# Kernel tuning notes

Measured on AMD Instinct MI355X. Metric: run time of the kernel, lower is better.

The kernel has to match this reference:

```python
import jax, jax.numpy as jnp
import numpy as np

S, E, H, V = 2048, 1024, 1024, 32000


def setup_inputs() -> dict:
    key = jax.random.key(0)
    ks = jax.random.split(key, 12)
    def n(k, shape, s=0.02):
        return jax.random.normal(k, shape, dtype=jnp.float32) * s
    return {
        "encoder_out": n(ks[0], (S, E), 1.0),
        "word_input": jax.random.randint(ks[1], (1,), 0, V),
        "last_context": n(ks[2], (1, H), 1.0),
        "h0": jnp.zeros((1, 1, H), jnp.float32),
        "c0": jnp.zeros((1, 1, H), jnp.float32),
        "emb": n(ks[3], (V, E)),
        "W_ih": n(ks[4], (4 * H, E + H)),
        "b_ih": jnp.zeros((4 * H,), jnp.float32),
        "W_hh": n(ks[5], (4 * H, H)),
        "b_hh": jnp.zeros((4 * H,), jnp.float32),
        "W_att": n(ks[6], (H, E + H)),
        "b_att": jnp.zeros((H,), jnp.float32),
        "v": jax.random.uniform(ks[7], (H,), dtype=jnp.float32) * 0.1,
        "W_ah": n(ks[8], (H, E + H)),
        "b_ah": jnp.zeros((H,), jnp.float32),
        "W_out": n(ks[9], (V, H)),
        "b_out": jnp.zeros((V,), jnp.float32),
    }


def reference(encoder_out, word_input, last_context, h0, c0, emb,
              W_ih, b_ih, W_hh, b_hh, W_att, b_att, v, W_ah, b_ah,
              W_out, b_out):
    # --- single LSTM step (torch gate order: i, f, g, o) ---
    x_emb = emb[word_input[0]]                         # [E]
    lstm_in = jnp.concatenate([last_context[0], x_emb])  # [E+H]
    gates = W_ih @ lstm_in + b_ih + W_hh @ h0[0, 0] + b_hh  # [4H]
    i, f, g, o = jnp.split(gates, 4)
    i = jax.nn.sigmoid(i); f = jax.nn.sigmoid(f)
    g = jnp.tanh(g);       o = jax.nn.sigmoid(o)
    c = f * c0[0, 0] + i * g                           # [H]
    h = o * jnp.tanh(c)                                # [H] (dropout: eval = identity)

    # --- batched additive (Bahdanau-style) attention over all S steps ---
    cat = jnp.concatenate([jnp.broadcast_to(h[None, :], (S, H)), encoder_out], axis=1)  # [S, H+E]
    scores = jnp.tanh(cat @ W_att.T + b_att) @ v       # [S]
    w = jax.nn.softmax(scores)                         # [S]
    context = w @ encoder_out                          # [E]

    # --- output projection ---
    x_t = jnp.tanh(W_ah @ jnp.concatenate([context, h]) + b_ah)  # [H]
    output = jax.nn.log_softmax(W_out @ x_t + b_out)[None, :]    # [1, V]
    return (output, (h[None, None, :], c[None, None, :]), x_t[None, :], w[None, :])
```

## Files before the change

kernel.cpp:

```cpp
#include <hip/hip_runtime.h>
#include <math.h>

typedef unsigned short u16;
typedef unsigned int u32;

typedef float  floatx4 __attribute__((ext_vector_type(4)));
typedef short  shortx8 __attribute__((ext_vector_type(8)));

#define S_LEN 2048
#define E_DIM 1024
#define H_DIM 1024
#define V_DIM 32000

#define OUT_LOG 0
#define OUT_H   32000
#define OUT_C   33024
#define OUT_XT  34048
#define OUT_W   35072

#define WS_UB     0
#define WS_SCORES 1024
#define WS_CTX    3072
#define WS_EXPSUM 4097
#define WS_ENC16  4608
#define WS_W16    (4608 + 1048576)

__device__ __forceinline__ u16 f2bf_fast(float f) {
    union { float f; u32 i; } v; v.f = f;
    return (u16)((v.i + 0x8000u) >> 16);
}
__device__ __forceinline__ float red16_sum(float x) {
    #pragma unroll
    for (int m = 1; m <= 8; m <<= 1) x += __shfl_xor(x, m, 64);
    return x;
}
__device__ __forceinline__ float wave_sum(float x) {
    #pragma unroll
    for (int m = 32; m >= 1; m >>= 1) x += __shfl_xor(x, m, 64);
    return x;
}
__device__ __forceinline__ float wave_max(float x) {
    #pragma unroll
    for (int m = 32; m >= 1; m >>= 1) x = fmaxf(x, __shfl_xor(x, m, 64));
    return x;
}
__device__ __forceinline__ float dot4(float4 a, float4 b) {
    return a.x * b.x + a.y * b.y + a.z * b.z + a.w * b.w;
}
__device__ __forceinline__ void cvt8(u16* t, float4 a, float4 b) {
    t[0] = f2bf_fast(a.x); t[1] = f2bf_fast(a.y);
    t[2] = f2bf_fast(a.z); t[3] = f2bf_fast(a.w);
    t[4] = f2bf_fast(b.x); t[5] = f2bf_fast(b.y);
    t[6] = f2bf_fast(b.z); t[7] = f2bf_fast(b.w);
}

__global__ __launch_bounds__(256) void k_lstm(
    const float* __restrict__ last_ctx, const int* __restrict__ word,
    const float* __restrict__ emb, const float* __restrict__ h0,
    const float* __restrict__ c0,
    const float* __restrict__ W_ih, const float* __restrict__ b_ih,
    const float* __restrict__ W_hh, const float* __restrict__ b_hh,
    float* __restrict__ out_h, float* __restrict__ out_c)
{
    __shared__ float gsh[4];
    int tid = threadIdx.x;
    int g = tid >> 6, l = tid & 63;
    int j = blockIdx.x;
    int row = g * H_DIM + j;
    const float* embrow = emb + (size_t)word[0] * E_DIM;
    const float* wrow = W_ih + (size_t)row * (E_DIM + H_DIM);
    const float* hrow = W_hh + (size_t)row * H_DIM;
    int c4 = l * 4;

    float s = 0.f;
    #pragma unroll
    for (int it = 0; it < 4; ++it) {
        int col = it * 256 + c4;
        s += dot4(*(const float4*)(wrow + col), *(const float4*)(last_ctx + col));
    }
    #pragma unroll
    for (int it = 0; it < 4; ++it) {
        int col = it * 256 + c4;
        s += dot4(*(const float4*)(wrow + 1024 + col), *(const float4*)(embrow + col));
    }
    #pragma unroll
    for (int it = 0; it < 4; ++it) {
        int col = it * 256 + c4;
        s += dot4(*(const float4*)(hrow + col), *(const float4*)(h0 + col));
    }
    s = wave_sum(s);
    if (l == 0) gsh[g] = s + b_ih[row] + b_hh[row];
    __syncthreads();
    if (tid == 0) {
        float gi = 1.f / (1.f + expf(-gsh[0]));
        float gf = 1.f / (1.f + expf(-gsh[1]));
        float gg = tanhf(gsh[2]);
        float go = 1.f / (1.f + expf(-gsh[3]));
        float c = gf * c0[j] + gi * gg;
        float h = go * tanhf(c);
        out_h[j] = h;
        out_c[j] = c;
    }
}

__global__ __launch_bounds__(256) void k_uproj(
    const float* __restrict__ W_att, const float* __restrict__ b_att,
    const float* __restrict__ out_h, const float* __restrict__ enc,
    float* __restrict__ wsf)
{
    int tid = threadIdx.x;
    int b = blockIdx.x;
    int gid = b * 256 + tid;
    if (gid < S_LEN) wsf[WS_SCORES + gid] = 0.f;
    else if (gid < S_LEN + E_DIM) wsf[WS_CTX + gid - S_LEN] = 0.f;
    else if (gid == S_LEN + E_DIM) wsf[WS_EXPSUM] = 0.f;

    int w = tid >> 6, l = tid & 63;
    int r = b * 4 + w;
    const float* wrow = W_att + (size_t)r * (E_DIM + H_DIM);
    int c4 = l * 4;
    float s = 0.f;
    #pragma unroll
    for (int it = 0; it < 4; ++it) {
        int col = it * 256 + c4;
        s += dot4(*(const float4*)(wrow + col), *(const float4*)(out_h + col));
    }
    s = wave_sum(s);
    if (l == 0) wsf[WS_UB + r] = s + b_att[r];

    u16* enc16 = (u16*)(wsf + WS_ENC16);
    u16* w16   = (u16*)(wsf + WS_W16);
    {
        int row = b * 8 + (tid >> 5);
        int col = (tid & 31) * 32;
        const float* src = enc + (size_t)row * E_DIM + col;
        u16 t[32];
        #pragma unroll
        for (int m = 0; m < 32; m += 8) {
            float4 x = *(const float4*)(src + m);
            float4 y = *(const float4*)(src + m + 4);
            cvt8(t + m, x, y);
        }
        uint4* dst = (uint4*)(enc16 + (size_t)row * E_DIM + col);
        #pragma unroll
        for (int m = 0; m < 4; ++m) dst[m] = *(uint4*)(t + m * 8);
    }
    {
        int row = b * 4 + (tid >> 6);
        int col = (tid & 63) * 16;
        const float* src = W_att + (size_t)row * (E_DIM + H_DIM) + H_DIM + col;
        u16 t[16];
        float4 x0 = *(const float4*)(src);
        float4 x1 = *(const float4*)(src + 4);
        float4 x2 = *(const float4*)(src + 8);
        float4 x3 = *(const float4*)(src + 12);
        cvt8(t, x0, x1); cvt8(t + 8, x2, x3);
        uint4* dst = (uint4*)(w16 + (size_t)row * E_DIM + col);
        dst[0] = *(uint4*)(t);
        dst[1] = *(uint4*)(t + 8);
    }
}

#define LDS_P 40
__global__ __launch_bounds__(256) void k_att_scores(
    const u16* __restrict__ enc16, const u16* __restrict__ w16,
    const float* __restrict__ vvec, const float* __restrict__ ws_ub,
    float* __restrict__ ws_scores)
{
    __shared__ u16 lds_a[2][64 * LDS_P];
    __shared__ u16 lds_b[2][64 * LDS_P];

    int tid = threadIdx.x;
    int w = tid >> 6, l = tid & 63;
    int b = blockIdx.x;
    int s0 = (b & 31) * 64;
    int r0 = (b >> 5) * 64;
    int lrow = l & 15, lq = l >> 4;

    int half = tid >> 7;
    int t128 = tid & 127;
    int srow = t128 >> 1;
    int scol = (t128 & 1) * 16;
    const u16* pbase = half == 0
        ? enc16 + (size_t)(s0 + srow) * E_DIM + scol
        : w16   + (size_t)(r0 + srow) * E_DIM + scol;
    u16* dst[2];
    dst[0] = half == 0 ? &lds_a[0][srow * LDS_P + scol] : &lds_b[0][srow * LDS_P + scol];
    dst[1] = half == 0 ? &lds_a[1][srow * LDS_P + scol] : &lds_b[1][srow * LDS_P + scol];

    floatx4 acc[4];
    #pragma unroll
    for (int i = 0; i < 4; ++i) acc[i] = (floatx4)0.f;

    {
        uint4 v0 = *(const uint4*)(pbase);
        uint4 v1 = *(const uint4*)(pbase + 8);
        *(uint4*)(dst[0])     = v0;
        *(uint4*)(dst[0] + 8) = v1;
    }
    __syncthreads();

    int cur = 0;
    for (int kc = 0; kc < 32; ++kc) {
        uint4 n0, n1;
        if (kc < 31) {
            const u16* p = pbase + (kc + 1) * 32;
            n0 = *(const uint4*)(p);
            n1 = *(const uint4*)(p + 8);
        }

        shortx8 afrag = *(const shortx8*)&lds_a[cur][(w * 16 + lrow) * LDS_P + lq * 8];
        #pragma unroll
        for (int rc = 0; rc < 4; ++rc) {
            shortx8 bfrag = *(const shortx8*)&lds_b[cur][(rc * 16 + lrow) * LDS_P + lq * 8];
            acc[rc] = __builtin_amdgcn_mfma_f32_16x16x32_bf16(afrag, bfrag, acc[rc], 0, 0, 0);
        }

        if (kc < 31) {
            int nb = cur ^ 1;
            *(uint4*)(dst[nb])     = n0;
            *(uint4*)(dst[nb] + 8) = n1;
        }
        __syncthreads();
        cur ^= 1;
    }

    float part[4] = {0.f, 0.f, 0.f, 0.f};
    #pragma unroll
    for (int rc = 0; rc < 4; ++rc) {
        int r = r0 + rc * 16 + lrow;
        float ubr = ws_ub[r];
        float vr  = vvec[r];
        #pragma unroll
        for (int reg = 0; reg < 4; ++reg)
            part[reg] += tanhf(acc[rc][reg] + ubr) * vr;
    }
    #pragma unroll
    for (int m = 1; m <= 8; m <<= 1)
        #pragma unroll
        for (int reg = 0; reg < 4; ++reg)
            part[reg] += __shfl_xor(part[reg], m, 64);
    if (lrow == 0) {
        int sbase = s0 + w * 16 + lq * 4;
        #pragma unroll
        for (int reg = 0; reg < 4; ++reg)
            atomicAdd(&ws_scores[sbase + reg], part[reg]);
    }
}

__global__ __launch_bounds__(256) void k_ctx(
    const float* __restrict__ enc, const float* __restrict__ ws_scores,
    float* __restrict__ out_w, float* __restrict__ ws_ctx)
{
    __shared__ float red[4];
    __shared__ float w_lds[16];
    __shared__ float bM, bS;
    int tid = threadIdx.x, b = blockIdx.x;

    float4 sa = *(const float4*)(ws_scores + tid * 8);
    float4 sb = *(const float4*)(ws_scores + tid * 8 + 4);
    float m = fmaxf(fmaxf(fmaxf(sa.x, sa.y), fmaxf(sa.z, sa.w)),
                    fmaxf(fmaxf(sb.x, sb.y), fmaxf(sb.z, sb.w)));
    m = wave_max(m);
    if ((tid & 63) == 0) red[tid >> 6] = m;
    __syncthreads();
    if (tid == 0) bM = fmaxf(fmaxf(red[0], red[1]), fmaxf(red[2], red[3]));
    __syncthreads();
    float M = bM;
    float e = expf(sa.x - M) + expf(sa.y - M) + expf(sa.z - M) + expf(sa.w - M)
            + expf(sb.x - M) + expf(sb.y - M) + expf(sb.z - M) + expf(sb.w - M);
    e = wave_sum(e);
    if ((tid & 63) == 0) red[tid >> 6] = e;
    __syncthreads();
    if (tid == 0) bS = red[0] + red[1] + red[2] + red[3];
    __syncthreads();
    float inv = 1.f / bS;

    int sbase = b * 16;
    if (tid < 16) {
        float wt = expf(ws_scores[sbase + tid] - M) * inv;
        w_lds[tid] = wt;
        out_w[sbase + tid] = wt;
    }
    __syncthreads();

    int e4 = tid * 4;
    float a0 = 0.f, a1 = 0.f, a2 = 0.f, a3 = 0.f;
    #pragma unroll 4
    for (int i = 0; i < 16; ++i) {
        float wt = w_lds[i];
        float4 ev = *(const float4*)(enc + (size_t)(sbase + i) * E_DIM + e4);
        a0 += wt * ev.x; a1 += wt * ev.y; a2 += wt * ev.z; a3 += wt * ev.w;
    }
    atomicAdd(&ws_ctx[e4 + 0], a0);
    atomicAdd(&ws_ctx[e4 + 1], a1);
    atomicAdd(&ws_ctx[e4 + 2], a2);
    atomicAdd(&ws_ctx[e4 + 3], a3);
}

__global__ __launch_bounds__(256) void k_xt(
    const float* __restrict__ W_ah, const float* __restrict__ b_ah,
    const float* __restrict__ ws_ctx, const float* __restrict__ out_h,
    float* __restrict__ out_xt)
{
    int tid = threadIdx.x;
    int w = tid >> 6, l = tid & 63;
    int r = blockIdx.x * 4 + w;
    const float* wrow = W_ah + (size_t)r * (E_DIM + H_DIM);
    int c4 = l * 4;
    float s = 0.f;
    #pragma unroll
    for (int it = 0; it < 4; ++it) {
        int col = it * 256 + c4;
        s += dot4(*(const float4*)(wrow + col), *(const float4*)(ws_ctx + col));
        s += dot4(*(const float4*)(wrow + 1024 + col), *(const float4*)(out_h + col));
    }
    s = wave_sum(s);
    if (l == 0) out_xt[r] = tanhf(s + b_ah[r]);
}

__global__ __launch_bounds__(256) void k_logits(
    const float* __restrict__ W_out, const float* __restrict__ b_out,
    const float* __restrict__ out_xt,
    float* __restrict__ out_log, float* __restrict__ ws_expsum)
{
    __shared__ float red[4];
    int tid = threadIdx.x;
    int w = tid >> 6, l = tid & 63;
    int sub = l >> 4, l16 = l & 15;
    int row = blockIdx.x * 16 + w * 4 + sub;
    const float* wrow = W_out + (size_t)row * H_DIM;
    int c4 = l16 * 4;
    float s = 0.f;
    #pragma unroll 4
    for (int it = 0; it < 16; ++it) {
        int col = it * 64 + c4;
        s += dot4(*(const float4*)(wrow + col), *(const float4*)(out_xt + col));
    }
    s = red16_sum(s);
    float lg = s + b_out[row];
    float e = 0.f;
    if (l16 == 0) { out_log[row] = lg; e = expf(lg); }
    e = wave_sum(e);
    if (l == 0) red[w] = e;
    __syncthreads();
    if (tid == 0)
        atomicAdd(ws_expsum, red[0] + red[1] + red[2] + red[3]);
}

__global__ __launch_bounds__(256) void k_writeout(
    const float* __restrict__ ws_expsum, float* __restrict__ out_log)
{
    int i = blockIdx.x * 256 + threadIdx.x;
    float lz = logf(ws_expsum[0]);
    out_log[i] = out_log[i] - lz;
}

extern "C" void kernel_launch(void* const* d_in, const int* in_sizes, int n_in,
                              void* d_out, int out_size, void* d_ws, size_t ws_size,
                              hipStream_t stream) {
    const float* enc      = (const float*)d_in[0];
    const int*   word     = (const int*)d_in[1];
    const float* last_ctx = (const float*)d_in[2];
    const float* h0       = (const float*)d_in[3];
    const float* c0       = (const float*)d_in[4];
    const float* emb      = (const float*)d_in[5];
    const float* W_ih     = (const float*)d_in[6];
    const float* b_ih     = (const float*)d_in[7];
    const float* W_hh     = (const float*)d_in[8];
    const float* b_hh     = (const float*)d_in[9];
    const float* W_att    = (const float*)d_in[10];
    const float* b_att    = (const float*)d_in[11];
    const float* vvec     = (const float*)d_in[12];
    const float* W_ah     = (const float*)d_in[13];
    const float* b_ah     = (const float*)d_in[14];
    const float* W_out    = (const float*)d_in[15];
    const float* b_out    = (const float*)d_in[16];

    float* wsf = (float*)d_ws;

    float* out     = (float*)d_out;
    float* out_log = out + OUT_LOG;
    float* out_h   = out + OUT_H;
    float* out_c   = out + OUT_C;
    float* out_xt  = out + OUT_XT;
    float* out_w   = out + OUT_W;

    k_lstm<<<1024, 256, 0, stream>>>(last_ctx, word, emb, h0, c0,
                                     W_ih, b_ih, W_hh, b_hh, out_h, out_c);
    k_uproj<<<256, 256, 0, stream>>>(W_att, b_att, out_h, enc, wsf);
    k_att_scores<<<512, 256, 0, stream>>>((const u16*)(wsf + WS_ENC16),
                                          (const u16*)(wsf + WS_W16),
                                          vvec, wsf + WS_UB, wsf + WS_SCORES);
    k_ctx<<<128, 256, 0, stream>>>(enc, wsf + WS_SCORES, out_w, wsf + WS_CTX);
    k_xt<<<256, 256, 0, stream>>>(W_ah, b_ah, wsf + WS_CTX, out_h, out_xt);
    k_logits<<<2000, 256, 0, stream>>>(W_out, b_out, out_xt,
                                       out_log, wsf + WS_EXPSUM);
    k_writeout<<<125, 256, 0, stream>>>(wsf + WS_EXPSUM, out_log);
}
```

Measured before the change: 360.0 us.

## Move bf16 conversion into LSTM kernel and replace score atomics with partial buffers

The fp32-to-bf16 conversion of encoder_out and the W_att encoder slice moves from k_uproj into k_lstm, spreading it across 1024 blocks that are already reading weights. In k_att_scores, the per-row-block score partials are written to a [16, S] buffer instead of being accumulated with atomicAdd. k_ctx then sums the 16 partials itself, which also removes the need to zero the scores buffer. This trades atomic contention for extra partial-buffer reads in every k_ctx block.

```diff
diff --git a/kernel.cpp b/kernel.cpp
--- a/kernel.cpp
+++ b/kernel.cpp
@@ -19,11 +19,11 @@
 #define OUT_W   35072
 
 #define WS_UB     0
-#define WS_SCORES 1024
-#define WS_CTX    3072
-#define WS_EXPSUM 4097
-#define WS_ENC16  4608
-#define WS_W16    (4608 + 1048576)
+#define WS_CTX    1024
+#define WS_EXPSUM 2048
+#define WS_PART   2560
+#define WS_ENC16  35840
+#define WS_W16    (35840 + 1048576)
 
 __device__ __forceinline__ u16 f2bf_fast(float f) {
     union { float f; u32 i; } v; v.f = f;
@@ -60,7 +60,9 @@
     const float* __restrict__ c0,
     const float* __restrict__ W_ih, const float* __restrict__ b_ih,
     const float* __restrict__ W_hh, const float* __restrict__ b_hh,
-    float* __restrict__ out_h, float* __restrict__ out_c)
+    const float* __restrict__ W_att, const float* __restrict__ enc,
+    float* __restrict__ out_h, float* __restrict__ out_c,
+    float* __restrict__ wsf)
 {
     __shared__ float gsh[4];
     int tid = threadIdx.x;
@@ -90,6 +92,29 @@
     }
     s = wave_sum(s);
     if (l == 0) gsh[g] = s + b_ih[row] + b_hh[row];
+
+    u16* enc16 = (u16*)(wsf + WS_ENC16);
+    u16* w16   = (u16*)(wsf + WS_W16);
+    {
+        int prow = 2 * j + (tid >> 7);
+        int pcol = (tid & 127) * 8;
+        const float* src = enc + (size_t)prow * E_DIM + pcol;
+        float4 x = *(const float4*)(src);
+        float4 y = *(const float4*)(src + 4);
+        u16 t[8];
+        cvt8(t, x, y);
+        *(uint4*)(enc16 + (size_t)prow * E_DIM + pcol) = *(uint4*)t;
+    }
+    {
+        int pcol = tid * 4;
+        const float* src = W_att + (size_t)j * (E_DIM + H_DIM) + H_DIM + pcol;
+        float4 x = *(const float4*)(src);
+        u16 t[4];
+        t[0] = f2bf_fast(x.x); t[1] = f2bf_fast(x.y);
+        t[2] = f2bf_fast(x.z); t[3] = f2bf_fast(x.w);
+        *(uint2*)(w16 + (size_t)j * E_DIM + pcol) = *(uint2*)t;
+    }
+
     __syncthreads();
     if (tid == 0) {
         float gi = 1.f / (1.f + expf(-gsh[0]));
@@ -105,15 +130,13 @@
 
 __global__ __launch_bounds__(256) void k_uproj(
     const float* __restrict__ W_att, const float* __restrict__ b_att,
-    const float* __restrict__ out_h, const float* __restrict__ enc,
-    float* __restrict__ wsf)
+    const float* __restrict__ out_h, float* __restrict__ wsf)
 {
     int tid = threadIdx.x;
     int b = blockIdx.x;
     int gid = b * 256 + tid;
-    if (gid < S_LEN) wsf[WS_SCORES + gid] = 0.f;
-    else if (gid < S_LEN + E_DIM) wsf[WS_CTX + gid - S_LEN] = 0.f;
-    else if (gid == S_LEN + E_DIM) wsf[WS_EXPSUM] = 0.f;
+    if (gid < E_DIM) wsf[WS_CTX + gid] = 0.f;
+    else if (gid == E_DIM) wsf[WS_EXPSUM] = 0.f;
 
     int w = tid >> 6, l = tid & 63;
     int r = b * 4 + w;
@@ -127,45 +150,13 @@
     }
     s = wave_sum(s);
     if (l == 0) wsf[WS_UB + r] = s + b_att[r];
-
-    u16* enc16 = (u16*)(wsf + WS_ENC16);
-    u16* w16   = (u16*)(wsf + WS_W16);
-    {
-        int row = b * 8 + (tid >> 5);
-        int col = (tid & 31) * 32;
-        const float* src = enc + (size_t)row * E_DIM + col;
-        u16 t[32];
-        #pragma unroll
-        for (int m = 0; m < 32; m += 8) {
-            float4 x = *(const float4*)(src + m);
-            float4 y = *(const float4*)(src + m + 4);
-            cvt8(t + m, x, y);
-        }
-        uint4* dst = (uint4*)(enc16 + (size_t)row * E_DIM + col);
-        #pragma unroll
-        for (int m = 0; m < 4; ++m) dst[m] = *(uint4*)(t + m * 8);
-    }
-    {
-        int row = b * 4 + (tid >> 6);
-        int col = (tid & 63) * 16;
-        const float* src = W_att + (size_t)row * (E_DIM + H_DIM) + H_DIM + col;
-        u16 t[16];
-        float4 x0 = *(const float4*)(src);
-        float4 x1 = *(const float4*)(src + 4);
-        float4 x2 = *(const float4*)(src + 8);
-        float4 x3 = *(const float4*)(src + 12);
-        cvt8(t, x0, x1); cvt8(t + 8, x2, x3);
-        uint4* dst = (uint4*)(w16 + (size_t)row * E_DIM + col);
-        dst[0] = *(uint4*)(t);
-        dst[1] = *(uint4*)(t + 8);
-    }
 }
 
 #define LDS_P 40
 __global__ __launch_bounds__(256) void k_att_scores(
     const u16* __restrict__ enc16, const u16* __restrict__ w16,
     const float* __restrict__ vvec, const float* __restrict__ ws_ub,
-    float* __restrict__ ws_scores)
+    float* __restrict__ ws_part)
 {
     __shared__ u16 lds_a[2][64 * LDS_P];
     __shared__ u16 lds_b[2][64 * LDS_P];
@@ -241,15 +232,16 @@
         for (int reg = 0; reg < 4; ++reg)
             part[reg] += __shfl_xor(part[reg], m, 64);
     if (lrow == 0) {
+        int rb = b >> 5;
         int sbase = s0 + w * 16 + lq * 4;
         #pragma unroll
         for (int reg = 0; reg < 4; ++reg)
-            atomicAdd(&ws_scores[sbase + reg], part[reg]);
+            ws_part[rb * S_LEN + sbase + reg] = part[reg];
     }
 }
 
 __global__ __launch_bounds__(256) void k_ctx(
-    const float* __restrict__ enc, const float* __restrict__ ws_scores,
+    const float* __restrict__ enc, const float* __restrict__ ws_part,
     float* __restrict__ out_w, float* __restrict__ ws_ctx)
 {
     __shared__ float red[4];
@@ -257,8 +249,17 @@
     __shared__ float bM, bS;
     int tid = threadIdx.x, b = blockIdx.x;
 
-    float4 sa = *(const float4*)(ws_scores + tid * 8);
-    float4 sb = *(const float4*)(ws_scores + tid * 8 + 4);
+    float4 sa = {0.f, 0.f, 0.f, 0.f};
+    float4 sb = {0.f, 0.f, 0.f, 0.f};
+    #pragma unroll
+    for (int rb = 0; rb < 16; ++rb) {
+        const float* p = ws_part + rb * S_LEN + tid * 8;
+        float4 a = *(const float4*)(p);
+        float4 c = *(const float4*)(p + 4);
+        sa.x += a.x; sa.y += a.y; sa.z += a.z; sa.w += a.w;
+        sb.x += c.x; sb.y += c.y; sb.z += c.z; sb.w += c.w;
+    }
+
     float m = fmaxf(fmaxf(fmaxf(sa.x, sa.y), fmaxf(sa.z, sa.w)),
                     fmaxf(fmaxf(sb.x, sb.y), fmaxf(sb.z, sb.w)));
     m = wave_max(m);
@@ -277,10 +278,15 @@
     float inv = 1.f / bS;
 
     int sbase = b * 16;
-    if (tid < 16) {
-        float wt = expf(ws_scores[sbase + tid] - M) * inv;
-        w_lds[tid] = wt;
-        out_w[sbase + tid] = wt;
+    if ((tid >> 1) == b) {
+        int off = (tid & 1) * 8;
+        float sc[8] = {sa.x, sa.y, sa.z, sa.w, sb.x, sb.y, sb.z, sb.w};
+        #pragma unroll
+        for (int i = 0; i < 8; ++i) {
+            float wt = expf(sc[i] - M) * inv;
+            w_lds[off + i] = wt;
+            out_w[sbase + off + i] = wt;
+        }
     }
     __syncthreads();
 
@@ -387,12 +393,13 @@
     float* out_w   = out + OUT_W;
 
     k_lstm<<<1024, 256, 0, stream>>>(last_ctx, word, emb, h0, c0,
-                                     W_ih, b_ih, W_hh, b_hh, out_h, out_c);
-    k_uproj<<<256, 256, 0, stream>>>(W_att, b_att, out_h, enc, wsf);
+                                     W_ih, b_ih, W_hh, b_hh, W_att, enc,
+                                     out_h, out_c, wsf);
+    k_uproj<<<256, 256, 0, stream>>>(W_att, b_att, out_h, wsf);
     k_att_scores<<<512, 256, 0, stream>>>((const u16*)(wsf + WS_ENC16),
                                           (const u16*)(wsf + WS_W16),
-                                          vvec, wsf + WS_UB, wsf + WS_SCORES);
-    k_ctx<<<128, 256, 0, stream>>>(enc, wsf + WS_SCORES, out_w, wsf + WS_CTX);
+                                          vvec, wsf + WS_UB, wsf + WS_PART);
+    k_ctx<<<128, 256, 0, stream>>>(enc, wsf + WS_PART, out_w, wsf + WS_CTX);
     k_xt<<<256, 256, 0, stream>>>(W_ah, b_ah, wsf + WS_CTX, out_h, out_xt);
     k_logits<<<2000, 256, 0, stream>>>(W_out, b_out, out_xt,
                                        out_log, wsf + WS_EXPSUM);
```

After: 358.1 us. Within noise of the previous version (-0.5%).
